# Kernel tuning notes

Measured on AMD Instinct MI355X. Metric: run time of the kernel, lower is better.

The kernel has to match this reference:

```python
import jax, jax.numpy as jnp
import numpy as np

B, N, D, H = 8, 1024, 512, 8
DH = D // H


def setup_inputs() -> dict:
    key = jax.random.key(0)
    ks = jax.random.split(key, 7)
    s = 1.0 / np.sqrt(D)
    return {
        "x": jax.random.normal(ks[0], (B, N, D), dtype=jnp.float32),
        "Wq": jax.random.normal(ks[1], (D, D), dtype=jnp.float32) * s,
        "bq": jax.random.normal(ks[2], (D,), dtype=jnp.float32) * 0.01,
        "Wk": jax.random.normal(ks[3], (D, D), dtype=jnp.float32) * s,
        "bk": jax.random.normal(ks[4], (D,), dtype=jnp.float32) * 0.01,
        "Wv": jax.random.normal(ks[5], (D, D), dtype=jnp.float32) * s,
        "bv": jax.random.normal(ks[6], (D,), dtype=jnp.float32) * 0.01,
    }


def reference(x, Wq, bq, Wk, bk, Wv, bv):
    # Q/K/V projections (nn.Linear: x @ W^T + b; here W stored as [in, out])
    q = x @ Wq + bq  # [B, N, D]
    k = x @ Wk + bk
    v = x @ Wv + bv
    # chunk(dim=2)+cat(dim=0) == split channels into H head groups
    q = q.reshape(B, N, H, DH)
    k = k.reshape(B, N, H, DH)
    v = v.reshape(B, N, H, DH)
    # NOTE: original applies NO 1/sqrt(head_dim) scaling
    scores = jnp.einsum("bqhd,bkhd->bhqk", q, k)  # [B, H, N, N]
    weights = jax.nn.softmax(scores, axis=-1)
    y = jnp.einsum("bhqk,bkhd->bqhd", weights, v)  # [B, N, H, DH]
    return y.reshape(B, N, D)
```

## Files before the change

### kernel.cpp

```cpp
#include <hip/hip_runtime.h>
#include <hip/hip_bf16.h>

typedef _Float16 half8 __attribute__((ext_vector_type(8)));
typedef _Float16 half4v __attribute__((ext_vector_type(4)));
typedef float floatx4 __attribute__((ext_vector_type(4)));

#define BB 8
#define NN 1024
#define DD 512
#define HH 8
#define DHH 64

__device__ __forceinline__ void gload_lds16(const _Float16* g, _Float16* l) {
    __builtin_amdgcn_global_load_lds(
        (const __attribute__((address_space(1))) void*)g,
        (__attribute__((address_space(3))) void*)l, 16, 0, 0);
}

__global__ __launch_bounds__(256) void cvt_kernel(const float* __restrict__ x,
                                                  const float* __restrict__ Wq,
                                                  const float* __restrict__ Wk,
                                                  const float* __restrict__ Wv,
                                                  _Float16* __restrict__ xh,
                                                  _Float16* __restrict__ Wt) {
    __shared__ __align__(16) _Float16 tb[64][72];
    int bx = blockIdx.x;
    int tid = threadIdx.x;
    if (bx < 4096) {
        int i = bx * 256 + tid;
        float4 v = ((const float4*)x)[i];
        half4v o;
        o[0] = (_Float16)v.x; o[1] = (_Float16)v.y;
        o[2] = (_Float16)v.z; o[3] = (_Float16)v.w;
        ((half4v*)xh)[i] = o;
        return;
    }
    int t = bx - 4096;
    int which = t >> 6;
    int rem = t & 63;
    int kt = (rem >> 3) * 64, nt = (rem & 7) * 64;
    const float* W = (which == 0) ? Wq : (which == 1) ? Wk : Wv;
    _Float16* Wto = Wt + (size_t)which * DD * DD;
    for (int i = 0; i < 16; i++) {
        int idx = tid + i * 256;
        int r = idx >> 6, c = idx & 63;
        tb[c][r] = (_Float16)W[(size_t)(kt + r) * DD + nt + c];
    }
    __syncthreads();
    for (int i = 0; i < 16; i++) {
        int idx = tid + i * 256;
        int r = idx >> 6, c = idx & 63;
        Wto[(size_t)(nt + r) * DD + kt + c] = tb[r][c];
    }
}

__global__ __launch_bounds__(256) void qkv_gemm_kernel(const _Float16* __restrict__ xh,
                                                       const _Float16* __restrict__ Wt,
                                                       const float* __restrict__ bq,
                                                       const float* __restrict__ bk,
                                                       const float* __restrict__ bv,
                                                       _Float16* __restrict__ QKV) {
    __shared__ __align__(16) _Float16 As[128 * 32];
    __shared__ __align__(16) _Float16 Bs[128 * 32];

    int which = blockIdx.z;
    const _Float16* Wtw = Wt + (size_t)which * DD * DD;
    const float* bias = (which == 0) ? bq : (which == 1) ? bk : bv;

    int tid = threadIdx.x;
    int wave = tid >> 6, lane = tid & 63;
    int quad = lane >> 4, l16 = lane & 15;
    int wm = wave >> 1, wn = wave & 1;
    int mBase = blockIdx.y * 128;
    int nBase = blockIdx.x * 128;

    int srow = wave * 32 + (lane >> 2);
    int scol = (lane & 3) * 8;
    const _Float16* ag = (which < 2)
        ? Wtw + (size_t)(nBase + srow) * DD + scol
        : xh  + (size_t)(mBase + srow) * DD + scol;
    const _Float16* bg = (which < 2)
        ? xh  + (size_t)(mBase + srow) * DD + scol
        : Wtw + (size_t)(nBase + srow) * DD + scol;
    _Float16* al = As + (wave * 32) * 32;
    _Float16* bl = Bs + (wave * 32) * 32;

    floatx4 acc[4][4];
    for (int i = 0; i < 4; i++)
        for (int j = 0; j < 4; j++) acc[i][j] = (floatx4){0.f, 0.f, 0.f, 0.f};

    for (int kk = 0; kk < DD; kk += 32) {
        __syncthreads();
        gload_lds16(ag + kk,            al);
        gload_lds16(ag + 16 * DD + kk,  al + 16 * 32);
        gload_lds16(bg + kk,            bl);
        gload_lds16(bg + 16 * DD + kk,  bl + 16 * 32);
        __syncthreads();

        half8 af[4], bf[4];
        for (int i = 0; i < 4; i++)
            af[i] = *(const half8*)&As[(wm * 64 + i * 16 + l16) * 32 + quad * 8];
        for (int j = 0; j < 4; j++)
            bf[j] = *(const half8*)&Bs[(wn * 64 + j * 16 + l16) * 32 + quad * 8];
        for (int i = 0; i < 4; i++)
            for (int j = 0; j < 4; j++)
                acc[i][j] = __builtin_amdgcn_mfma_f32_16x16x32_f16(af[i], bf[j], acc[i][j], 0, 0, 0);
    }

    if (which < 2) {
        _Float16* out = QKV + (size_t)which * (BB * NN) * DD;
        for (int i = 0; i < 4; i++) {
            int feat0 = nBase + wm * 64 + i * 16 + quad * 4;
            float4 b4 = *(const float4*)&bias[feat0];
            for (int j = 0; j < 4; j++) {
                int token = mBase + wn * 64 + j * 16 + l16;
                half4v pack;
                pack[0] = (_Float16)(acc[i][j][0] + b4.x);
                pack[1] = (_Float16)(acc[i][j][1] + b4.y);
                pack[2] = (_Float16)(acc[i][j][2] + b4.z);
                pack[3] = (_Float16)(acc[i][j][3] + b4.w);
                *(half4v*)&out[(size_t)token * DD + feat0] = pack;
            }
        }
    } else {
        _Float16* VT = QKV + (size_t)2 * (BB * NN) * DD;
        for (int j = 0; j < 4; j++) {
            int col = nBase + wn * 64 + j * 16 + l16;
            float bval = bias[col];
            for (int i = 0; i < 4; i++) {
                int row0 = mBase + wm * 64 + i * 16 + quad * 4;
                int b = row0 >> 10;
                int n = row0 & 1023;
                half4v pack;
                for (int reg = 0; reg < 4; reg++) pack[reg] = (_Float16)(acc[i][j][reg] + bval);
                *(half4v*)&VT[((size_t)b * 512 + col) * 1024 + n] = pack;
            }
        }
    }
}

__global__ __launch_bounds__(256) void attn_kernel(const _Float16* __restrict__ QKV,
                                                   float* __restrict__ out) {
    const _Float16* Q  = QKV;
    const _Float16* K  = QKV + (size_t)(BB * NN) * DD;
    const _Float16* VT = QKV + (size_t)2 * (BB * NN) * DD;

    __shared__ __align__(16) _Float16 Kt[128 * 64];
    __shared__ __align__(16) _Float16 Vt[64 * 128];
    __shared__ __align__(16) _Float16 PT[4][16 * 64];

    int tid = threadIdx.x;
    int wave = tid >> 6, lane = tid & 63;
    int quad = lane >> 4, l16 = lane & 15;
    int qt = blockIdx.x, h = blockIdx.y, b = blockIdx.z;

    const _Float16* Qb  = Q + ((size_t)b * NN) * DD + h * DHH;
    const _Float16* Kb  = K + ((size_t)b * NN) * DD + h * DHH;
    const _Float16* VTb = VT + ((size_t)b * 512 + h * 64) * 1024;

    int qrow = qt * 64 + wave * 16 + l16;
    half8 qf0 = *(const half8*)(Qb + (size_t)qrow * DD + 0 * 32 + quad * 8);
    half8 qf1 = *(const half8*)(Qb + (size_t)qrow * DD + 1 * 32 + quad * 8);

    floatx4 o[4];
    for (int nt = 0; nt < 4; nt++) o[nt] = (floatx4){0.f, 0.f, 0.f, 0.f};
    float m_i = -1e30f, l_i = 0.f;

    const _Float16* kg = Kb + (size_t)(wave * 32 + (lane >> 3)) * DD
                            + ((lane & 7) ^ (lane >> 3)) * 8;
    _Float16* kl = Kt + (wave * 32) * 64;
    _Float16* vl = Vt + (wave * 16) * 128;
    int l16sw = l16 & 7;

    for (int kt = 0; kt < 8; kt++) {
        __syncthreads();
        for (int i = 0; i < 4; i++)
            gload_lds16(kg + (size_t)(kt * 128 + i * 8) * DD, kl + (i * 8) * 64);
        for (int i = 0; i < 4; i++) {
            int vrow = wave * 16 + i * 4 + (lane >> 4);
            int vc = (lane & 15) ^ (i * 4 + (lane >> 4));
            gload_lds16(VTb + (size_t)vrow * 1024 + kt * 128 + vc * 8, vl + (i * 4) * 128);
        }
        __syncthreads();

        floatx4 s[8];
        for (int nt = 0; nt < 8; nt++) s[nt] = (floatx4){0.f, 0.f, 0.f, 0.f};
        for (int ks = 0; ks < 2; ks++) {
            half8 qf = ks ? qf1 : qf0;
            for (int nt = 0; nt < 8; nt++) {
                half8 kf = *(const half8*)&Kt[(nt * 16 + l16) * 64
                                              + (((ks * 4 + quad) ^ l16sw) * 8)];
                s[nt] = __builtin_amdgcn_mfma_f32_16x16x32_f16(kf, qf, s[nt], 0, 0, 0);
            }
        }

        float mx = -1e30f;
        for (int nt = 0; nt < 8; nt++)
            for (int r = 0; r < 4; r++) mx = fmaxf(mx, s[nt][r]);
        mx = fmaxf(mx, __shfl_xor(mx, 16, 64));
        mx = fmaxf(mx, __shfl_xor(mx, 32, 64));
        float mnew = fmaxf(m_i, mx);
        float alpha = __expf(m_i - mnew);
        m_i = mnew;
        float rs = 0.f;
        for (int nt = 0; nt < 8; nt++)
            for (int r = 0; r < 4; r++) {
                float p = __expf(s[nt][r] - mnew);
                s[nt][r] = p;
                rs += p;
            }
        rs += __shfl_xor(rs, 16, 64);
        rs += __shfl_xor(rs, 32, 64);
        l_i = l_i * alpha + rs;

        for (int nt = 0; nt < 4; nt++)
            for (int r = 0; r < 4; r++) o[nt][r] *= alpha;

        for (int hh = 0; hh < 2; hh++) {
            for (int ntl = 0; ntl < 4; ntl++) {
                floatx4 sv = s[hh * 4 + ntl];
                half4v p4;
                for (int r = 0; r < 4; r++) p4[r] = (_Float16)sv[r];
                *(half4v*)&PT[wave][l16 * 64 + (((2 * ntl + (quad >> 1)) ^ l16sw) * 8)
                               + (quad & 1) * 4] = p4;
            }
            for (int ks2h = 0; ks2h < 2; ks2h++) {
                half8 pf = *(const half8*)&PT[wave][l16 * 64
                                                   + (((ks2h * 4 + quad) ^ l16sw) * 8)];
                int ks2 = hh * 2 + ks2h;
                for (int nt = 0; nt < 4; nt++) {
                    half8 vf = *(const half8*)&Vt[(nt * 16 + l16) * 128
                                                  + (((ks2 * 4 + quad) ^ l16) * 8)];
                    o[nt] = __builtin_amdgcn_mfma_f32_16x16x32_f16(vf, pf, o[nt], 0, 0, 0);
                }
            }
        }
    }

    float inv = 1.0f / l_i;
    float* outb = out + ((size_t)b * NN) * DD + h * DHH;
    int row = qt * 64 + wave * 16 + l16;
    for (int nt = 0; nt < 4; nt++) {
        float4 st;
        st.x = o[nt][0] * inv; st.y = o[nt][1] * inv;
        st.z = o[nt][2] * inv; st.w = o[nt][3] * inv;
        *(float4*)&outb[(size_t)row * DD + nt * 16 + quad * 4] = st;
    }
}

extern "C" void kernel_launch(void* const* d_in, const int* in_sizes, int n_in,
                              void* d_out, int out_size, void* d_ws, size_t ws_size,
                              hipStream_t stream) {
    const float* x  = (const float*)d_in[0];
    const float* Wq = (const float*)d_in[1];
    const float* bq = (const float*)d_in[2];
    const float* Wk = (const float*)d_in[3];
    const float* bk = (const float*)d_in[4];
    const float* Wv = (const float*)d_in[5];
    const float* bv = (const float*)d_in[6];
    float* out = (float*)d_out;

    _Float16* xh  = (_Float16*)d_ws;
    _Float16* Wt  = xh + (size_t)(BB * NN) * DD;
    _Float16* QKV = Wt + (size_t)3 * DD * DD;

    hipLaunchKernelGGL(cvt_kernel, dim3(4096 + 192), dim3(256), 0, stream,
                       x, Wq, Wk, Wv, xh, Wt);
    hipLaunchKernelGGL(qkv_gemm_kernel, dim3(4, 64, 3), dim3(256), 0, stream,
                       xh, Wt, bq, bk, bv, QKV);
    hipLaunchKernelGGL(attn_kernel, dim3(16, 8, 8), dim3(256), 0, stream, QKV, out);
}
```

Measured before the change: 142.0 us.

## Double-buffer x tile in QKV GEMM, load weights directly, reorder attention grid

The QKV GEMM now stages only the x tile in LDS, double-buffered so the next k-slice is fetched while the current one feeds MFMA, with one barrier per iteration instead of two. Weight fragments are read straight from global memory into registers, with no LDS staging. The attention kernel grid is reordered so the head index varies fastest, which changes which blocks run together and how they share cache. The P-to-fp16 conversion now uses packed round-toward-zero conversion instructions. Uncached direct weight loads may add global latency, and round-toward-zero slightly changes rounding.

```diff
diff --git a/kernel.cpp b/kernel.cpp
--- a/kernel.cpp
+++ b/kernel.cpp
@@ -60,8 +60,7 @@
                                                        const float* __restrict__ bk,
                                                        const float* __restrict__ bv,
                                                        _Float16* __restrict__ QKV) {
-    __shared__ __align__(16) _Float16 As[128 * 32];
-    __shared__ __align__(16) _Float16 Bs[128 * 32];
+    __shared__ __align__(16) _Float16 Bs[2][128 * 32];
 
     int which = blockIdx.z;
     const _Float16* Wtw = Wt + (size_t)which * DD * DD;
@@ -76,35 +75,48 @@
 
     int srow = wave * 32 + (lane >> 2);
     int scol = (lane & 3) * 8;
-    const _Float16* ag = (which < 2)
-        ? Wtw + (size_t)(nBase + srow) * DD + scol
-        : xh  + (size_t)(mBase + srow) * DD + scol;
-    const _Float16* bg = (which < 2)
-        ? xh  + (size_t)(mBase + srow) * DD + scol
-        : Wtw + (size_t)(nBase + srow) * DD + scol;
-    _Float16* al = As + (wave * 32) * 32;
-    _Float16* bl = Bs + (wave * 32) * 32;
+    const _Float16* bg = xh + (size_t)(mBase + srow) * DD + scol;
+    _Float16* bl[2] = { Bs[0] + (wave * 32) * 32, Bs[1] + (wave * 32) * 32 };
+
+    int xw = (which < 2) ? wn : wm;
+    int ww = (which < 2) ? wm : wn;
+    const _Float16* wbase = Wtw + (size_t)(nBase + ww * 64 + l16) * DD + quad * 8;
 
     floatx4 acc[4][4];
     for (int i = 0; i < 4; i++)
         for (int j = 0; j < 4; j++) acc[i][j] = (floatx4){0.f, 0.f, 0.f, 0.f};
 
-    for (int kk = 0; kk < DD; kk += 32) {
+    gload_lds16(bg, bl[0]);
+    gload_lds16(bg + 16 * DD, bl[0] + 16 * 32);
+    __syncthreads();
+
+    for (int kt = 0; kt < 16; kt++) {
+        int cur = kt & 1;
+        if (kt < 15) {
+            int kk = (kt + 1) * 32;
+            gload_lds16(bg + kk, bl[cur ^ 1]);
+            gload_lds16(bg + 16 * DD + kk, bl[cur ^ 1] + 16 * 32);
+        }
+        int kk = kt * 32;
+
+        half8 wf[4], xf[4];
+        for (int t = 0; t < 4; t++)
+            wf[t] = *(const half8*)(wbase + (size_t)(t * 16) * DD + kk);
+        for (int t = 0; t < 4; t++)
+            xf[t] = *(const half8*)&Bs[cur][(xw * 64 + t * 16 + l16) * 32 + quad * 8];
+
+        if (which < 2) {
+            for (int i = 0; i < 4; i++)
+                for (int j = 0; j < 4; j++)
+                    acc[i][j] = __builtin_amdgcn_mfma_f32_16x16x32_f16(wf[i], xf[j],
+                                                                       acc[i][j], 0, 0, 0);
+        } else {
+            for (int i = 0; i < 4; i++)
+                for (int j = 0; j < 4; j++)
+                    acc[i][j] = __builtin_amdgcn_mfma_f32_16x16x32_f16(xf[i], wf[j],
+                                                                       acc[i][j], 0, 0, 0);
+        }
         __syncthreads();
-        gload_lds16(ag + kk,            al);
-        gload_lds16(ag + 16 * DD + kk,  al + 16 * 32);
-        gload_lds16(bg + kk,            bl);
-        gload_lds16(bg + 16 * DD + kk,  bl + 16 * 32);
-        __syncthreads();
-
-        half8 af[4], bf[4];
-        for (int i = 0; i < 4; i++)
-            af[i] = *(const half8*)&As[(wm * 64 + i * 16 + l16) * 32 + quad * 8];
-        for (int j = 0; j < 4; j++)
-            bf[j] = *(const half8*)&Bs[(wn * 64 + j * 16 + l16) * 32 + quad * 8];
-        for (int i = 0; i < 4; i++)
-            for (int j = 0; j < 4; j++)
-                acc[i][j] = __builtin_amdgcn_mfma_f32_16x16x32_f16(af[i], bf[j], acc[i][j], 0, 0, 0);
     }
 
     if (which < 2) {
@@ -152,7 +164,7 @@
     int tid = threadIdx.x;
     int wave = tid >> 6, lane = tid & 63;
     int quad = lane >> 4, l16 = lane & 15;
-    int qt = blockIdx.x, h = blockIdx.y, b = blockIdx.z;
+    int h = blockIdx.x, qt = blockIdx.y, b = blockIdx.z;
 
     const _Float16* Qb  = Q + ((size_t)b * NN) * DD + h * DHH;
     const _Float16* Kb  = K + ((size_t)b * NN) * DD + h * DHH;
@@ -219,10 +231,10 @@
         for (int hh = 0; hh < 2; hh++) {
             for (int ntl = 0; ntl < 4; ntl++) {
                 floatx4 sv = s[hh * 4 + ntl];
-                half4v p4;
-                for (int r = 0; r < 4; r++) p4[r] = (_Float16)sv[r];
-                *(half4v*)&PT[wave][l16 * 64 + (((2 * ntl + (quad >> 1)) ^ l16sw) * 8)
-                               + (quad & 1) * 4] = p4;
+                int d0 = __builtin_bit_cast(int, __builtin_amdgcn_cvt_pkrtz(sv[0], sv[1]));
+                int d1 = __builtin_bit_cast(int, __builtin_amdgcn_cvt_pkrtz(sv[2], sv[3]));
+                *(int2*)&PT[wave][l16 * 64 + (((2 * ntl + (quad >> 1)) ^ l16sw) * 8)
+                               + (quad & 1) * 4] = make_int2(d0, d1);
             }
             for (int ks2h = 0; ks2h < 2; ks2h++) {
                 half8 pf = *(const half8*)&PT[wave][l16 * 64
@@ -268,5 +280,5 @@
                        x, Wq, Wk, Wv, xh, Wt);
     hipLaunchKernelGGL(qkv_gemm_kernel, dim3(4, 64, 3), dim3(256), 0, stream,
                        xh, Wt, bq, bk, bv, QKV);
-    hipLaunchKernelGGL(attn_kernel, dim3(16, 8, 8), dim3(256), 0, stream, QKV, out);
-}
+    hipLaunchKernelGGL(attn_kernel, dim3(8, 16, 8), dim3(256), 0, stream, QKV, out);
+}
```

Result: slower. 158.9 us (+11.9%).
